# Kernel tuning notes

Hardware: AMD Instinct MI355X
Metric: run time of the kernel (lower is better)

## Reference

```python
import jax, jax.numpy as jnp
import numpy as np

NUM_HEADS = 8
HEAD_SIZE = 64


def setup_inputs() -> dict:
    key = jax.random.key(0)
    ks = jax.random.split(key, 7)
    B, P, De, F = 16, 64, 512, 128
    d_model = NUM_HEADS * HEAD_SIZE  # 512
    s = 0.05  # ~ keras RandomNormal default stddev
    return {
        "patch_embeddings": jax.random.normal(ks[0], (B, P, De), jnp.float32),
        "patches_relative_feature": jax.random.normal(ks[1], (B, P, P, F), jnp.float32),
        "patches_relative_mask": jnp.ones((B, P, P), dtype=bool),
        "Wq": jax.random.normal(ks[2], (De, d_model), jnp.float32) * s,
        "Wk": jax.random.normal(ks[3], (De + F, d_model), jnp.float32) * s,
        "Wv": jax.random.normal(ks[4], (De + F, d_model), jnp.float32) * s,
        "Wo": jax.random.normal(ks[5], (d_model, d_model), jnp.float32) * s,
    }


def reference(patch_embeddings, patches_relative_feature, patches_relative_mask, Wq, Wk, Wv, Wo):
    # Vectorized form of the per-patch python loop: for query patch q,
    # keys/values come from concat(patch_embeddings, rel_feature[:, q]).
    B, P, De = patch_embeddings.shape
    H, hs = NUM_HEADS, HEAD_SIZE
    q = (patch_embeddings @ Wq).reshape(B, P, H, hs)  # [B,P,H,hs], seq_len=1 per patch
    # relative key/value inputs: [B, Pq, Pk, De+F]
    rel = jnp.concatenate(
        [jnp.broadcast_to(patch_embeddings[:, None], (B, P, P, De)), patches_relative_feature],
        axis=-1,
    )
    k = (rel @ Wk).reshape(B, P, P, H, hs)
    v = (rel @ Wv).reshape(B, P, P, H, hs)
    scale = 1.0 / jnp.sqrt(jnp.asarray(hs, q.dtype))
    scores = jnp.einsum("bqhd,bqkhd->bqhk", q, k) * scale  # [B,Pq,H,Pk]
    attn = jax.nn.softmax(scores, axis=-1)
    out = jnp.einsum("bqhk,bqkhd->bqhd", attn, v).reshape(B, P, H * hs)
    return out @ Wo  # [B, P, d_model]
```

## Files before the change

### kernel.cpp

```cpp
#include <hip/hip_runtime.h>
#include <hip/hip_bf16.h>


typedef __attribute__((ext_vector_type(8))) short short8;
typedef __attribute__((ext_vector_type(4))) short short4v;
typedef __attribute__((ext_vector_type(4))) float f32x4;

static __device__ __forceinline__ short f2bf(float x) {
  __hip_bfloat16 h = __float2bfloat16(x);
  union { __hip_bfloat16 h; short s; } u;
  u.h = h;
  return u.s;
}
static __device__ __forceinline__ float bf2f(short s) {
  union { unsigned int u; float f; } c;
  c.u = ((unsigned int)(unsigned short)s) << 16;
  return c.f;
}
static __device__ __forceinline__ float bflo(unsigned int u) {
  union { unsigned int u; float f; } c; c.u = u << 16; return c.f;
}
static __device__ __forceinline__ float bfhi(unsigned int u) {
  union { unsigned int u; float f; } c; c.u = u & 0xFFFF0000u; return c.f;
}
static __device__ __forceinline__ short8 ldcvt(const float* p) {
  float4 v0 = *(const float4*)p, v1 = *(const float4*)(p + 4);
  short8 r = {f2bf(v0.x), f2bf(v0.y), f2bf(v0.z), f2bf(v0.w),
              f2bf(v1.x), f2bf(v1.y), f2bf(v1.z), f2bf(v1.w)};
  return r;
}

__global__ __launch_bounds__(256) void prep(const float* __restrict__ Wq,
                                            const float* __restrict__ Wk,
                                            const float* __restrict__ Wv,
                                            const float* __restrict__ Wo,
                                            short* __restrict__ Bt,
                                            short* __restrict__ BtO,
                                            short* __restrict__ Wk2t,
                                            short* __restrict__ Wv2bf) {
  __shared__ float t[32][33];
  const int bid = blockIdx.x, tid = threadIdx.x;
  if (bid < 1024) {
    const int np0 = (bid & 63) * 32, k0 = (bid >> 6) * 32;
    const int tx = tid & 31, ty = tid >> 5;
    const int sid = np0 >> 9;
    const float* src = (sid == 0) ? Wq : (sid == 1) ? Wv : (sid == 2) ? Wk : Wo;
    const int nc0 = np0 & 511;
#pragma unroll
    for (int r = 0; r < 4; ++r) {
      int kl = ty + r * 8;
      t[kl][tx] = src[(size_t)(k0 + kl) * 512 + nc0 + tx];
    }
    __syncthreads();
#pragma unroll
    for (int r = 0; r < 4; ++r) {
      int nl = ty + r * 8;
      short bv = f2bf(t[tx][nl]);
      int np = np0 + nl;
      if (np < 1536) Bt[(size_t)np * 512 + k0 + tx] = bv;
      else           BtO[(size_t)(np - 1536) * 512 + k0 + tx] = bv;
    }
  } else if (bid < 1088) {
    const int b2 = bid - 1024;
    const int f0 = (b2 & 3) * 32, e0 = (b2 >> 2) * 32;
    const int tx = tid & 31, ty = tid >> 5;
    const float* Wk2 = Wk + 512 * 512;
#pragma unroll
    for (int r = 0; r < 4; ++r) {
      int fl = ty + r * 8;
      t[fl][tx] = Wk2[(size_t)(f0 + fl) * 512 + e0 + tx];
    }
    __syncthreads();
#pragma unroll
    for (int r = 0; r < 4; ++r) {
      int el = ty + r * 8;
      Wk2t[(size_t)(e0 + el) * 128 + f0 + tx] = f2bf(t[tx][el]);
    }
  } else {
    int i = ((bid - 1088) * 256 + tid) * 4;
    const float* Wv2 = Wv + 512 * 512;
    float4 v = *(const float4*)(Wv2 + i);
    short4v o = {f2bf(v.x), f2bf(v.y), f2bf(v.z), f2bf(v.w)};
    *(short4v*)(Wv2bf + i) = o;
  }
}

__global__ __launch_bounds__(256) void gemm_qkvu(const float* __restrict__ A,
                                                 const short* __restrict__ Bt,
                                                 short* __restrict__ QV,
                                                 short* __restrict__ K0t2) {
  const int wave = threadIdx.x >> 6, lane = threadIdx.x & 63;
  const int wr = wave >> 1, wc = wave & 1;
  const int r = lane & 15, g = lane >> 4;
  const int row0 = blockIdx.x * 64 + wr * 32;
  const int col0 = blockIdx.y * 64 + wc * 32;
  const float* a0f = A + (size_t)(row0 + r) * 512 + g * 8;
  const float* a1f = A + (size_t)(row0 + 16 + r) * 512 + g * 8;
  const short8* b0p = (const short8*)(Bt + (size_t)(col0 + r) * 512 + g * 8);
  const short8* b1p = (const short8*)(Bt + (size_t)(col0 + 16 + r) * 512 + g * 8);
  f32x4 acc00 = {}, acc01 = {}, acc10 = {}, acc11 = {};
  short8 A0[2][4], A1[2][4], B0[2][4], B1[2][4];
  auto LOAD = [&](int buf, int ss) {
#pragma unroll
    for (int c = 0; c < 4; ++c) {
      A0[buf][c] = ldcvt(a0f + (ss * 4 + c) * 32);
      A1[buf][c] = ldcvt(a1f + (ss * 4 + c) * 32);
      B0[buf][c] = b0p[(ss * 4 + c) * 4];
      B1[buf][c] = b1p[(ss * 4 + c) * 4];
    }
  };
  auto MM = [&](int buf) {
#pragma unroll
    for (int c = 0; c < 4; ++c) {
      acc00 = __builtin_amdgcn_mfma_f32_16x16x32_bf16(A0[buf][c], B0[buf][c], acc00, 0, 0, 0);
      acc01 = __builtin_amdgcn_mfma_f32_16x16x32_bf16(A0[buf][c], B1[buf][c], acc01, 0, 0, 0);
      acc10 = __builtin_amdgcn_mfma_f32_16x16x32_bf16(A1[buf][c], B0[buf][c], acc10, 0, 0, 0);
      acc11 = __builtin_amdgcn_mfma_f32_16x16x32_bf16(A1[buf][c], B1[buf][c], acc11, 0, 0, 0);
    }
  };
  LOAD(0, 0);
  LOAD(1, 1);
  MM(0);
  LOAD(0, 2);
  MM(1);
  LOAD(1, 3);
  MM(0);
  MM(1);
  const int crow = (lane >> 4) * 4, ccol = lane & 15;
  const bool k0sec = (blockIdx.y >= 16);
#pragma unroll
  for (int i = 0; i < 2; ++i)
#pragma unroll
    for (int j = 0; j < 2; ++j) {
      f32x4 a = (i == 0) ? (j == 0 ? acc00 : acc01) : (j == 0 ? acc10 : acc11);
#pragma unroll
      for (int rg = 0; rg < 4; ++rg) {
        size_t row = row0 + i * 16 + crow + rg;
        size_t col = col0 + j * 16 + ccol;
        short v = f2bf(a[rg]);
        if (!k0sec) {
          QV[row * 1024 + col] = v;
        } else {
          size_t c = col - 1024;
          size_t b = row >> 6, kk = row & 63;
          K0t2[((b * 256 + (c >> 1)) * 64 + kk) * 2 + (c & 1)] = v;
        }
      }
    }
}

__global__ __launch_bounds__(256) void gemm_out(const short* __restrict__ A,
                                                const short* __restrict__ Bt,
                                                float* __restrict__ C) {
  const int wave = threadIdx.x >> 6, lane = threadIdx.x & 63;
  const int wr = wave >> 1, wc = wave & 1;
  const int r = lane & 15, g = lane >> 4;
  const int row0 = blockIdx.x * 64 + wr * 32;
  const int col0 = blockIdx.y * 64 + wc * 32;
  const short8* a0p = (const short8*)(A + (size_t)(row0 + r) * 512 + g * 8);
  const short8* a1p = (const short8*)(A + (size_t)(row0 + 16 + r) * 512 + g * 8);
  const short8* b0p = (const short8*)(Bt + (size_t)(col0 + r) * 512 + g * 8);
  const short8* b1p = (const short8*)(Bt + (size_t)(col0 + 16 + r) * 512 + g * 8);
  f32x4 acc00 = {}, acc01 = {}, acc10 = {}, acc11 = {};
  short8 A0[2][4], A1[2][4], B0[2][4], B1[2][4];
  auto LOAD = [&](int buf, int ss) {
#pragma unroll
    for (int c = 0; c < 4; ++c) {
      A0[buf][c] = a0p[(ss * 4 + c) * 4];
      A1[buf][c] = a1p[(ss * 4 + c) * 4];
      B0[buf][c] = b0p[(ss * 4 + c) * 4];
      B1[buf][c] = b1p[(ss * 4 + c) * 4];
    }
  };
  auto MM = [&](int buf) {
#pragma unroll
    for (int c = 0; c < 4; ++c) {
      acc00 = __builtin_amdgcn_mfma_f32_16x16x32_bf16(A0[buf][c], B0[buf][c], acc00, 0, 0, 0);
      acc01 = __builtin_amdgcn_mfma_f32_16x16x32_bf16(A0[buf][c], B1[buf][c], acc01, 0, 0, 0);
      acc10 = __builtin_amdgcn_mfma_f32_16x16x32_bf16(A1[buf][c], B0[buf][c], acc10, 0, 0, 0);
      acc11 = __builtin_amdgcn_mfma_f32_16x16x32_bf16(A1[buf][c], B1[buf][c], acc11, 0, 0, 0);
    }
  };
  LOAD(0, 0);
  LOAD(1, 1);
  MM(0);
  LOAD(0, 2);
  MM(1);
  LOAD(1, 3);
  MM(0);
  MM(1);
  const int crow = (lane >> 4) * 4, ccol = lane & 15;
#pragma unroll
  for (int i = 0; i < 2; ++i)
#pragma unroll
    for (int j = 0; j < 2; ++j) {
      f32x4 a = (i == 0) ? (j == 0 ? acc00 : acc01) : (j == 0 ? acc10 : acc11);
#pragma unroll
      for (int rg = 0; rg < 4; ++rg)
        C[(size_t)(row0 + i * 16 + crow + rg) * 512 + col0 + j * 16 + ccol] = a[rg];
    }
}

__global__ __launch_bounds__(512) void attn_fused(const short* __restrict__ QV,
                                                  const unsigned int* __restrict__ K0t2,
                                                  const float* __restrict__ relf,
                                                  const short* __restrict__ Wk2t,
                                                  const short* __restrict__ Wv2bf,
                                                  short* __restrict__ AO) {
  const int orig = blockIdx.x;
  const int bq = (orig & 7) * 128 + (orig >> 3);
  const int b = bq >> 6;
  const int tid = threadIdx.x;
  const int h = tid >> 6, lane = tid & 63;

  __shared__ short relf_s[64][136];
  __shared__ float q_s[512];
  __shared__ float u_s[8][128];
  __shared__ float attn_s[8][64];
  __shared__ float w_s[8][128];

  q_s[tid] = bf2f(QV[(size_t)bq * 1024 + tid]);

  const float* rf = relf + (size_t)bq * 8192;
#pragma unroll
  for (int it = 0; it < 4; ++it) {
    int idx = (it * 512 + tid) * 4;
    float4 gv = *(const float4*)(rf + idx);
    int kk = idx >> 7, f = idx & 127;
    short4v o = {f2bf(gv.x), f2bf(gv.y), f2bf(gv.z), f2bf(gv.w)};
    *(short4v*)&relf_s[kk][f] = o;
  }
  __syncthreads();

  {
    const unsigned int* wp = (const unsigned int*)(Wk2t + (size_t)h * 64 * 128) + lane;
    float u0 = 0.f, u1 = 0.f;
#pragma unroll 8
    for (int d = 0; d < 64; ++d) {
      unsigned int uv = wp[d * 64];
      float qd = q_s[h * 64 + d];
      u0 += qd * bflo(uv);
      u1 += qd * bfhi(uv);
    }
    u_s[h][lane * 2] = u0;
    u_s[h][lane * 2 + 1] = u1;
  }

  float s = 0.f;
  {
    const unsigned int* kp = K0t2 + ((size_t)b * 256 + h * 32) * 64 + lane;
#pragma unroll 8
    for (int d2 = 0; d2 < 32; ++d2) {
      unsigned int uv = kp[(size_t)d2 * 64];
      s += q_s[h * 64 + d2 * 2] * bflo(uv) + q_s[h * 64 + d2 * 2 + 1] * bfhi(uv);
    }
#pragma unroll
    for (int f8 = 0; f8 < 16; ++f8) {
      short8 rv = *(const short8*)&relf_s[lane][f8 * 8];
      float4 ua = *(const float4*)&u_s[h][f8 * 8];
      float4 ub = *(const float4*)&u_s[h][f8 * 8 + 4];
      s += ua.x * bf2f(rv[0]) + ua.y * bf2f(rv[1]) + ua.z * bf2f(rv[2]) + ua.w * bf2f(rv[3]);
      s += ub.x * bf2f(rv[4]) + ub.y * bf2f(rv[5]) + ub.z * bf2f(rv[6]) + ub.w * bf2f(rv[7]);
    }
    s *= 0.125f;
  }
  float m = s;
#pragma unroll
  for (int off = 32; off; off >>= 1) m = fmaxf(m, __shfl_xor(m, off));
  float p = __expf(s - m);
  float sum = p;
#pragma unroll
  for (int off = 32; off; off >>= 1) sum += __shfl_xor(sum, off);
  attn_s[h][lane] = p / sum;

  {
    float w0 = 0.f, w1 = 0.f;
#pragma unroll 8
    for (int kk = 0; kk < 64; ++kk) {
      float a = attn_s[h][kk];
      w0 += a * bf2f(relf_s[kk][lane]);
      w1 += a * bf2f(relf_s[kk][lane + 64]);
    }
    w_s[h][lane] = w0;
    w_s[h][lane + 64] = w1;
  }

  float o = 0.f;
  {
    const short* v0col = QV + (size_t)(b * 64) * 1024 + 512 + h * 64 + lane;
#pragma unroll 16
    for (int kk = 0; kk < 64; ++kk) o += attn_s[h][kk] * bf2f(v0col[(size_t)kk * 1024]);
    const short* wvcol = Wv2bf + h * 64 + lane;
#pragma unroll 16
    for (int f = 0; f < 128; ++f) o += w_s[h][f] * bf2f(wvcol[(size_t)f * 512]);
  }
  AO[(size_t)bq * 512 + h * 64 + lane] = f2bf(o);
}

extern "C" void kernel_launch(void* const* d_in, const int* in_sizes, int n_in,
                              void* d_out, int out_size, void* d_ws, size_t ws_size,
                              hipStream_t stream) {
  const float* pe   = (const float*)d_in[0];
  const float* relf = (const float*)d_in[1];
  const float* Wq = (const float*)d_in[3];
  const float* Wk = (const float*)d_in[4];
  const float* Wv = (const float*)d_in[5];
  const float* Wo = (const float*)d_in[6];
  float* out = (float*)d_out;

  short* ws = (short*)d_ws;
  short* Bt    = ws;
  short* BtO   = Bt + 786432;
  short* Wk2t  = BtO + 262144;
  short* Wv2bf = Wk2t + 65536;
  short* QV    = Wv2bf + 65536;
  short* K0t2  = QV + 1048576;
  short* AObf  = K0t2 + 524288;

  prep<<<1152, 256, 0, stream>>>(Wq, Wk, Wv, Wo, Bt, BtO, Wk2t, Wv2bf);
  gemm_qkvu<<<dim3(16, 24), 256, 0, stream>>>(pe, Bt, QV, K0t2);
  attn_fused<<<1024, 512, 0, stream>>>(QV, (const unsigned int*)K0t2, relf, Wk2t, Wv2bf, AObf);
  gemm_out<<<dim3(16, 8), 256, 0, stream>>>(AObf, BtO, out);
}
```

Before: 147.1 us.

## Fuse all four stages into one cooperative persistent kernel with grid syncs

Replaces the four separate launches (weight prep, QKV GEMM, attention, output GEMM) with a single cooperative kernel of 256 blocks that runs each stage in grid-stride loops separated by grid.sync(). The aim is to remove launch overhead and inter-kernel gaps. In exchange it adds grid-wide barriers and gives the attention stage only 256 resident blocks, each looping over 4 queries. The fallback kernels' software-pipelined MFMA loops are also simplified into plain unrolled loops.

```diff
diff --git a/kernel.cpp b/kernel.cpp
--- a/kernel.cpp
+++ b/kernel.cpp
@@ -1,5 +1,8 @@
 #include <hip/hip_runtime.h>
 #include <hip/hip_bf16.h>
+#include <hip/hip_cooperative_groups.h>
+
+namespace cg = cooperative_groups;
 
 
 typedef __attribute__((ext_vector_type(8))) short short8;
@@ -28,6 +31,252 @@
   short8 r = {f2bf(v0.x), f2bf(v0.y), f2bf(v0.z), f2bf(v0.w),
               f2bf(v1.x), f2bf(v1.y), f2bf(v1.z), f2bf(v1.w)};
   return r;
+}
+static __device__ __forceinline__ f32x4 mfma_bf(short8 a, short8 b, f32x4 c) {
+  return __builtin_amdgcn_mfma_f32_16x16x32_bf16(a, b, c, 0, 0, 0);
+}
+
+#define WS_BT    0
+#define WS_BTO   786432
+#define WS_WK2T  (WS_BTO + 262144)
+#define WS_WV2   (WS_WK2T + 65536)
+#define WS_QV    (WS_WV2 + 65536)
+#define WS_K0T2  (WS_QV + 1048576)
+#define WS_AO    (WS_K0T2 + 524288)
+
+__global__ __launch_bounds__(512) void fused_all(const float* __restrict__ pe,
+                                                 const float* __restrict__ relf,
+                                                 const float* __restrict__ Wq,
+                                                 const float* __restrict__ Wk,
+                                                 const float* __restrict__ Wv,
+                                                 const float* __restrict__ Wo,
+                                                 float* __restrict__ out,
+                                                 short* __restrict__ ws) {
+  cg::grid_group grid = cg::this_grid();
+  const int bid = blockIdx.x, tid = threadIdx.x;
+
+  short* Bt    = ws + WS_BT;
+  short* BtO   = ws + WS_BTO;
+  short* Wk2t  = ws + WS_WK2T;
+  short* Wv2bf = ws + WS_WV2;
+  short* QV    = ws + WS_QV;
+  short* K0t2  = ws + WS_K0T2;
+  short* AObf  = ws + WS_AO;
+
+  __shared__ float t[32][33];
+  __shared__ short relf_s[64][136];
+  __shared__ float q_s[512];
+  __shared__ float u_s[8][128];
+  __shared__ float attn_s[8][64];
+  __shared__ float w_s[8][128];
+
+  {
+    const int tx = tid & 31, ty2 = tid >> 5;
+    for (int slot = bid; slot < 1120; slot += 256) {
+      if (slot < 1024) {
+        const int np0 = (slot & 63) * 32, k0 = (slot >> 6) * 32;
+        const int sid = np0 >> 9;
+        const float* src = (sid == 0) ? Wq : (sid == 1) ? Wv : (sid == 2) ? Wk : Wo;
+        const int nc0 = np0 & 511;
+#pragma unroll
+        for (int r = 0; r < 2; ++r) {
+          int kl = ty2 + r * 16;
+          t[kl][tx] = src[(size_t)(k0 + kl) * 512 + nc0 + tx];
+        }
+        __syncthreads();
+#pragma unroll
+        for (int r = 0; r < 2; ++r) {
+          int nl = ty2 + r * 16;
+          short bv = f2bf(t[tx][nl]);
+          int np = np0 + nl;
+          if (np < 1536) Bt[(size_t)np * 512 + k0 + tx] = bv;
+          else           BtO[(size_t)(np - 1536) * 512 + k0 + tx] = bv;
+        }
+        __syncthreads();
+      } else if (slot < 1088) {
+        const int b2 = slot - 1024;
+        const int f0 = (b2 & 3) * 32, e0 = (b2 >> 2) * 32;
+        const float* Wk2 = Wk + 512 * 512;
+#pragma unroll
+        for (int r = 0; r < 2; ++r) {
+          int fl = ty2 + r * 16;
+          t[fl][tx] = Wk2[(size_t)(f0 + fl) * 512 + e0 + tx];
+        }
+        __syncthreads();
+#pragma unroll
+        for (int r = 0; r < 2; ++r) {
+          int el = ty2 + r * 16;
+          Wk2t[(size_t)(e0 + el) * 128 + f0 + tx] = f2bf(t[tx][el]);
+        }
+        __syncthreads();
+      } else {
+        int i = ((slot - 1088) * 512 + tid) * 4;
+        const float* Wv2 = Wv + 512 * 512;
+        float4 v = *(const float4*)(Wv2 + i);
+        short4v o = {f2bf(v.x), f2bf(v.y), f2bf(v.z), f2bf(v.w)};
+        *(short4v*)(Wv2bf + i) = o;
+      }
+    }
+  }
+  grid.sync();
+
+  {
+    const int w = (tid >> 6) & 3, lane = tid & 63;
+    const int r = lane & 15, g = lane >> 4;
+#pragma unroll 1
+    for (int pass = 0; pass < 2; ++pass) {
+      const int unit = pass * 512 + bid * 2 + (tid >> 8);
+      if (unit < 768) {
+        const int m = unit & 31, n = unit >> 5;
+        const int row = m * 32 + (w & 1) * 16 + r;
+        const int col0 = n * 64 + (w >> 1) * 32;
+        const float* af = pe + (size_t)row * 512 + g * 8;
+        const short8* b0p = (const short8*)(Bt + (size_t)(col0 + r) * 512 + g * 8);
+        const short8* b1p = (const short8*)(Bt + (size_t)(col0 + 16 + r) * 512 + g * 8);
+        f32x4 acc0 = {}, acc1 = {};
+#pragma unroll 4
+        for (int tk = 0; tk < 16; ++tk) {
+          short8 a = ldcvt(af + tk * 32);
+          acc0 = mfma_bf(a, b0p[tk * 4], acc0);
+          acc1 = mfma_bf(a, b1p[tk * 4], acc1);
+        }
+        const int crow = (lane >> 4) * 4, ccol = lane & 15;
+#pragma unroll
+        for (int j = 0; j < 2; ++j) {
+          f32x4 fr = j ? acc1 : acc0;
+#pragma unroll
+          for (int rg = 0; rg < 4; ++rg) {
+            size_t orow = (size_t)m * 32 + (w & 1) * 16 + crow + rg;
+            size_t ocol = (size_t)col0 + j * 16 + ccol;
+            short v = f2bf(fr[rg]);
+            if (ocol < 1024) {
+              QV[orow * 1024 + ocol] = v;
+            } else {
+              size_t c = ocol - 1024;
+              K0t2[(((orow >> 6) * 256 + (c >> 1)) * 64 + (orow & 63)) * 2 + (c & 1)] = v;
+            }
+          }
+        }
+      }
+    }
+  }
+  grid.sync();
+
+  {
+    const int h = tid >> 6, lane = tid & 63;
+    const unsigned int* K0t2u = (const unsigned int*)K0t2;
+#pragma unroll 1
+    for (int it = 0; it < 4; ++it) {
+      const int bq = (bid & 7) * 128 + (bid >> 3) + it * 32;
+      const int b = bq >> 6;
+      __syncthreads();
+      q_s[tid] = bf2f(QV[(size_t)bq * 1024 + tid]);
+      const float* rf = relf + (size_t)bq * 8192;
+#pragma unroll
+      for (int i4 = 0; i4 < 4; ++i4) {
+        int idx = (i4 * 512 + tid) * 4;
+        float4 gv = *(const float4*)(rf + idx);
+        int kk = idx >> 7, f = idx & 127;
+        short4v o = {f2bf(gv.x), f2bf(gv.y), f2bf(gv.z), f2bf(gv.w)};
+        *(short4v*)&relf_s[kk][f] = o;
+      }
+      __syncthreads();
+
+      {
+        const unsigned int* wp = (const unsigned int*)(Wk2t + (size_t)h * 64 * 128) + lane;
+        float u0 = 0.f, u1 = 0.f;
+#pragma unroll 8
+        for (int d = 0; d < 64; ++d) {
+          unsigned int uv = wp[d * 64];
+          float qd = q_s[h * 64 + d];
+          u0 += qd * bflo(uv);
+          u1 += qd * bfhi(uv);
+        }
+        u_s[h][lane * 2] = u0;
+        u_s[h][lane * 2 + 1] = u1;
+      }
+
+      float s = 0.f;
+      {
+        const unsigned int* kp = K0t2u + ((size_t)b * 256 + h * 32) * 64 + lane;
+#pragma unroll 8
+        for (int d2 = 0; d2 < 32; ++d2) {
+          unsigned int uv = kp[(size_t)d2 * 64];
+          s += q_s[h * 64 + d2 * 2] * bflo(uv) + q_s[h * 64 + d2 * 2 + 1] * bfhi(uv);
+        }
+#pragma unroll
+        for (int f8 = 0; f8 < 16; ++f8) {
+          short8 rv = *(const short8*)&relf_s[lane][f8 * 8];
+          float4 ua = *(const float4*)&u_s[h][f8 * 8];
+          float4 ub = *(const float4*)&u_s[h][f8 * 8 + 4];
+          s += ua.x * bf2f(rv[0]) + ua.y * bf2f(rv[1]) + ua.z * bf2f(rv[2]) + ua.w * bf2f(rv[3]);
+          s += ub.x * bf2f(rv[4]) + ub.y * bf2f(rv[5]) + ub.z * bf2f(rv[6]) + ub.w * bf2f(rv[7]);
+        }
+        s *= 0.125f;
+      }
+      float mx = s;
+#pragma unroll
+      for (int off = 32; off; off >>= 1) mx = fmaxf(mx, __shfl_xor(mx, off));
+      float p = __expf(s - mx);
+      float sum = p;
+#pragma unroll
+      for (int off = 32; off; off >>= 1) sum += __shfl_xor(sum, off);
+      attn_s[h][lane] = p / sum;
+
+      {
+        float w0 = 0.f, w1 = 0.f;
+#pragma unroll 8
+        for (int kk = 0; kk < 64; ++kk) {
+          float a = attn_s[h][kk];
+          w0 += a * bf2f(relf_s[kk][lane]);
+          w1 += a * bf2f(relf_s[kk][lane + 64]);
+        }
+        w_s[h][lane] = w0;
+        w_s[h][lane + 64] = w1;
+      }
+
+      float o = 0.f;
+      {
+        const short* v0col = QV + (size_t)(b * 64) * 1024 + 512 + h * 64 + lane;
+#pragma unroll 16
+        for (int kk = 0; kk < 64; ++kk) o += attn_s[h][kk] * bf2f(v0col[(size_t)kk * 1024]);
+        const short* wvcol = Wv2bf + h * 64 + lane;
+#pragma unroll 16
+        for (int f = 0; f < 128; ++f) o += w_s[h][f] * bf2f(wvcol[(size_t)f * 512]);
+      }
+      AObf[(size_t)bq * 512 + h * 64 + lane] = f2bf(o);
+    }
+  }
+  grid.sync();
+
+  {
+    const int unit = bid * 2 + (tid >> 8);
+    if (unit < 256) {
+      const int w = (tid >> 6) & 3, lane = tid & 63;
+      const int m = unit & 31, n = unit >> 5;
+      const int r = lane & 15, g = lane >> 4;
+      const int row = m * 32 + (w & 1) * 16 + r;
+      const int col0 = n * 64 + (w >> 1) * 32;
+      const short8* ap = (const short8*)(AObf + (size_t)row * 512 + g * 8);
+      const short8* b0p = (const short8*)(BtO + (size_t)(col0 + r) * 512 + g * 8);
+      const short8* b1p = (const short8*)(BtO + (size_t)(col0 + 16 + r) * 512 + g * 8);
+      f32x4 acc0 = {}, acc1 = {};
+#pragma unroll 4
+      for (int tk = 0; tk < 16; ++tk) {
+        short8 a = ap[tk * 4];
+        acc0 = mfma_bf(a, b0p[tk * 4], acc0);
+        acc1 = mfma_bf(a, b1p[tk * 4], acc1);
+      }
+      const int crow = (lane >> 4) * 4, ccol = lane & 15;
+#pragma unroll
+      for (int j = 0; j < 2; ++j) {
+        f32x4 fr = j ? acc1 : acc0;
+#pragma unroll
+        for (int rg = 0; rg < 4; ++rg)
+          out[(size_t)(m * 32 + (w & 1) * 16 + crow + rg) * 512 + col0 + j * 16 + ccol] = fr[rg];
+      }
+    }
+  }
 }
 
 __global__ __launch_bounds__(256) void prep(const float* __restrict__ Wq,
@@ -99,33 +348,15 @@
   const short8* b0p = (const short8*)(Bt + (size_t)(col0 + r) * 512 + g * 8);
   const short8* b1p = (const short8*)(Bt + (size_t)(col0 + 16 + r) * 512 + g * 8);
   f32x4 acc00 = {}, acc01 = {}, acc10 = {}, acc11 = {};
-  short8 A0[2][4], A1[2][4], B0[2][4], B1[2][4];
-  auto LOAD = [&](int buf, int ss) {
-#pragma unroll
-    for (int c = 0; c < 4; ++c) {
-      A0[buf][c] = ldcvt(a0f + (ss * 4 + c) * 32);
-      A1[buf][c] = ldcvt(a1f + (ss * 4 + c) * 32);
-      B0[buf][c] = b0p[(ss * 4 + c) * 4];
-      B1[buf][c] = b1p[(ss * 4 + c) * 4];
-    }
-  };
-  auto MM = [&](int buf) {
-#pragma unroll
-    for (int c = 0; c < 4; ++c) {
-      acc00 = __builtin_amdgcn_mfma_f32_16x16x32_bf16(A0[buf][c], B0[buf][c], acc00, 0, 0, 0);
-      acc01 = __builtin_amdgcn_mfma_f32_16x16x32_bf16(A0[buf][c], B1[buf][c], acc01, 0, 0, 0);
-      acc10 = __builtin_amdgcn_mfma_f32_16x16x32_bf16(A1[buf][c], B0[buf][c], acc10, 0, 0, 0);
-      acc11 = __builtin_amdgcn_mfma_f32_16x16x32_bf16(A1[buf][c], B1[buf][c], acc11, 0, 0, 0);
-    }
-  };
-  LOAD(0, 0);
-  LOAD(1, 1);
-  MM(0);
-  LOAD(0, 2);
-  MM(1);
-  LOAD(1, 3);
-  MM(0);
-  MM(1);
+#pragma unroll 4
+  for (int t = 0; t < 16; ++t) {
+    short8 a0 = ldcvt(a0f + t * 32), a1 = ldcvt(a1f + t * 32);
+    short8 b0 = b0p[t * 4], b1 = b1p[t * 4];
+    acc00 = mfma_bf(a0, b0, acc00);
+    acc01 = mfma_bf(a0, b1, acc01);
+    acc10 = mfma_bf(a1, b0, acc10);
+    acc11 = mfma_bf(a1, b1, acc11);
+  }
   const int crow = (lane >> 4) * 4, ccol = lane & 15;
   const bool k0sec = (blockIdx.y >= 16);
 #pragma unroll
@@ -162,33 +393,15 @@
   const short8* b0p = (const short8*)(Bt + (size_t)(col0 + r) * 512 + g * 8);
   const short8* b1p = (const short8*)(Bt + (size_t)(col0 + 16 + r) * 512 + g * 8);
   f32x4 acc00 = {}, acc01 = {}, acc10 = {}, acc11 = {};
-  short8 A0[2][4], A1[2][4], B0[2][4], B1[2][4];
-  auto LOAD = [&](int buf, int ss) {
-#pragma unroll
-    for (int c = 0; c < 4; ++c) {
-      A0[buf][c] = a0p[(ss * 4 + c) * 4];
-      A1[buf][c] = a1p[(ss * 4 + c) * 4];
-      B0[buf][c] = b0p[(ss * 4 + c) * 4];
-      B1[buf][c] = b1p[(ss * 4 + c) * 4];
-    }
-  };
-  auto MM = [&](int buf) {
-#pragma unroll
-    for (int c = 0; c < 4; ++c) {
-      acc00 = __builtin_amdgcn_mfma_f32_16x16x32_bf16(A0[buf][c], B0[buf][c], acc00, 0, 0, 0);
-      acc01 = __builtin_amdgcn_mfma_f32_16x16x32_bf16(A0[buf][c], B1[buf][c], acc01, 0, 0, 0);
-      acc10 = __builtin_amdgcn_mfma_f32_16x16x32_bf16(A1[buf][c], B0[buf][c], acc10, 0, 0, 0);
-      acc11 = __builtin_amdgcn_mfma_f32_16x16x32_bf16(A1[buf][c], B1[buf][c], acc11, 0, 0, 0);
-    }
-  };
-  LOAD(0, 0);
-  LOAD(1, 1);
-  MM(0);
-  LOAD(0, 2);
-  MM(1);
-  LOAD(1, 3);
-  MM(0);
-  MM(1);
+#pragma unroll 4
+  for (int t = 0; t < 16; ++t) {
+    short8 a0 = a0p[t * 4], a1 = a1p[t * 4];
+    short8 b0 = b0p[t * 4], b1 = b1p[t * 4];
+    acc00 = mfma_bf(a0, b0, acc00);
+    acc01 = mfma_bf(a0, b1, acc01);
+    acc10 = mfma_bf(a1, b0, acc10);
+    acc11 = mfma_bf(a1, b1, acc11);
+  }
   const int crow = (lane >> 4) * 4, ccol = lane & 15;
 #pragma unroll
   for (int i = 0; i < 2; ++i)
@@ -220,7 +433,6 @@
   __shared__ float w_s[8][128];
 
   q_s[tid] = bf2f(QV[(size_t)bq * 1024 + tid]);
-
   const float* rf = relf + (size_t)bq * 8192;
 #pragma unroll
   for (int it = 0; it < 4; ++it) {
@@ -307,18 +519,23 @@
   const float* Wv = (const float*)d_in[5];
   const float* Wo = (const float*)d_in[6];
   float* out = (float*)d_out;
-
   short* ws = (short*)d_ws;
-  short* Bt    = ws;
-  short* BtO   = Bt + 786432;
-  short* Wk2t  = BtO + 262144;
-  short* Wv2bf = Wk2t + 65536;
-  short* QV    = Wv2bf + 65536;
-  short* K0t2  = QV + 1048576;
-  short* AObf  = K0t2 + 524288;
-
-  prep<<<1152, 256, 0, stream>>>(Wq, Wk, Wv, Wo, Bt, BtO, Wk2t, Wv2bf);
-  gemm_qkvu<<<dim3(16, 24), 256, 0, stream>>>(pe, Bt, QV, K0t2);
-  attn_fused<<<1024, 512, 0, stream>>>(QV, (const unsigned int*)K0t2, relf, Wk2t, Wv2bf, AObf);
-  gemm_out<<<dim3(16, 8), 256, 0, stream>>>(AObf, BtO, out);
-}
+
+  void* args[] = {(void*)&pe, (void*)&relf, (void*)&Wq, (void*)&Wk,
+                  (void*)&Wv, (void*)&Wo, (void*)&out, (void*)&ws};
+  hipError_t err = hipLaunchCooperativeKernel((const void*)fused_all, dim3(256), dim3(512),
+                                              args, 0, stream);
+  if (err != hipSuccess) {
+    short* Bt    = ws + WS_BT;
+    short* BtO   = ws + WS_BTO;
+    short* Wk2t  = ws + WS_WK2T;
+    short* Wv2bf = ws + WS_WV2;
+    short* QV    = ws + WS_QV;
+    short* K0t2  = ws + WS_K0T2;
+    short* AObf  = ws + WS_AO;
+    prep<<<1152, 256, 0, stream>>>(Wq, Wk, Wv, Wo, Bt, BtO, Wk2t, Wv2bf);
+    gemm_qkvu<<<dim3(16, 24), 256, 0, stream>>>(pe, Bt, QV, K0t2);
+    attn_fused<<<1024, 512, 0, stream>>>(QV, (const unsigned int*)K0t2, relf, Wk2t, Wv2bf, AObf);
+    gemm_out<<<dim3(16, 8), 256, 0, stream>>>(AObf, BtO, out);
+  }
+}
```

Result: slower. 277.1 us (+88.4%).

## Fuse output projection into attention kernel and keep relative features in fp32 LDS

Applied to the files above, without the earlier changes.

Drops the separate Wo transpose and MFMA output GEMM. Each attention block now multiplies its 512-wide attention output row by fp32 Wo directly, reading Wo from global memory column-wise. This removes one kernel launch and the bf16 AO round trip, but it re-reads Wo (1 MB) from every one of the 1024 blocks and does that GEMM on scalar FMAs instead of MFMA. Relative features are also stored as fp32 in padded LDS, with no bf16 conversion, and some accumulations are split into several partial sums for ILP.

```diff
diff --git a/kernel.cpp b/kernel.cpp
--- a/kernel.cpp
+++ b/kernel.cpp
@@ -29,22 +29,23 @@
               f2bf(v1.x), f2bf(v1.y), f2bf(v1.z), f2bf(v1.w)};
   return r;
 }
+static __device__ __forceinline__ f32x4 mfma_bf(short8 a, short8 b, f32x4 c) {
+  return __builtin_amdgcn_mfma_f32_16x16x32_bf16(a, b, c, 0, 0, 0);
+}
 
 __global__ __launch_bounds__(256) void prep(const float* __restrict__ Wq,
                                             const float* __restrict__ Wk,
                                             const float* __restrict__ Wv,
-                                            const float* __restrict__ Wo,
                                             short* __restrict__ Bt,
-                                            short* __restrict__ BtO,
                                             short* __restrict__ Wk2t,
                                             short* __restrict__ Wv2bf) {
   __shared__ float t[32][33];
   const int bid = blockIdx.x, tid = threadIdx.x;
-  if (bid < 1024) {
-    const int np0 = (bid & 63) * 32, k0 = (bid >> 6) * 32;
+  if (bid < 768) {
+    const int np0 = (bid % 48) * 32, k0 = (bid / 48) * 32;
     const int tx = tid & 31, ty = tid >> 5;
     const int sid = np0 >> 9;
-    const float* src = (sid == 0) ? Wq : (sid == 1) ? Wv : (sid == 2) ? Wk : Wo;
+    const float* src = (sid == 0) ? Wq : (sid == 1) ? Wv : Wk;
     const int nc0 = np0 & 511;
 #pragma unroll
     for (int r = 0; r < 4; ++r) {
@@ -55,13 +56,10 @@
 #pragma unroll
     for (int r = 0; r < 4; ++r) {
       int nl = ty + r * 8;
-      short bv = f2bf(t[tx][nl]);
-      int np = np0 + nl;
-      if (np < 1536) Bt[(size_t)np * 512 + k0 + tx] = bv;
-      else           BtO[(size_t)(np - 1536) * 512 + k0 + tx] = bv;
-    }
-  } else if (bid < 1088) {
-    const int b2 = bid - 1024;
+      Bt[(size_t)(np0 + nl) * 512 + k0 + tx] = f2bf(t[tx][nl]);
+    }
+  } else if (bid < 832) {
+    const int b2 = bid - 768;
     const int f0 = (b2 & 3) * 32, e0 = (b2 >> 2) * 32;
     const int tx = tid & 31, ty = tid >> 5;
     const float* Wk2 = Wk + 512 * 512;
@@ -77,7 +75,7 @@
       Wk2t[(size_t)(e0 + el) * 128 + f0 + tx] = f2bf(t[tx][el]);
     }
   } else {
-    int i = ((bid - 1088) * 256 + tid) * 4;
+    int i = ((bid - 832) * 256 + tid) * 4;
     const float* Wv2 = Wv + 512 * 512;
     float4 v = *(const float4*)(Wv2 + i);
     short4v o = {f2bf(v.x), f2bf(v.y), f2bf(v.z), f2bf(v.w)};
@@ -112,10 +110,10 @@
   auto MM = [&](int buf) {
 #pragma unroll
     for (int c = 0; c < 4; ++c) {
-      acc00 = __builtin_amdgcn_mfma_f32_16x16x32_bf16(A0[buf][c], B0[buf][c], acc00, 0, 0, 0);
-      acc01 = __builtin_amdgcn_mfma_f32_16x16x32_bf16(A0[buf][c], B1[buf][c], acc01, 0, 0, 0);
-      acc10 = __builtin_amdgcn_mfma_f32_16x16x32_bf16(A1[buf][c], B0[buf][c], acc10, 0, 0, 0);
-      acc11 = __builtin_amdgcn_mfma_f32_16x16x32_bf16(A1[buf][c], B1[buf][c], acc11, 0, 0, 0);
+      acc00 = mfma_bf(A0[buf][c], B0[buf][c], acc00);
+      acc01 = mfma_bf(A0[buf][c], B1[buf][c], acc01);
+      acc10 = mfma_bf(A1[buf][c], B0[buf][c], acc10);
+      acc11 = mfma_bf(A1[buf][c], B1[buf][c], acc11);
     }
   };
   LOAD(0, 0);
@@ -149,75 +147,25 @@
     }
 }
 
-__global__ __launch_bounds__(256) void gemm_out(const short* __restrict__ A,
-                                                const short* __restrict__ Bt,
-                                                float* __restrict__ C) {
-  const int wave = threadIdx.x >> 6, lane = threadIdx.x & 63;
-  const int wr = wave >> 1, wc = wave & 1;
-  const int r = lane & 15, g = lane >> 4;
-  const int row0 = blockIdx.x * 64 + wr * 32;
-  const int col0 = blockIdx.y * 64 + wc * 32;
-  const short8* a0p = (const short8*)(A + (size_t)(row0 + r) * 512 + g * 8);
-  const short8* a1p = (const short8*)(A + (size_t)(row0 + 16 + r) * 512 + g * 8);
-  const short8* b0p = (const short8*)(Bt + (size_t)(col0 + r) * 512 + g * 8);
-  const short8* b1p = (const short8*)(Bt + (size_t)(col0 + 16 + r) * 512 + g * 8);
-  f32x4 acc00 = {}, acc01 = {}, acc10 = {}, acc11 = {};
-  short8 A0[2][4], A1[2][4], B0[2][4], B1[2][4];
-  auto LOAD = [&](int buf, int ss) {
-#pragma unroll
-    for (int c = 0; c < 4; ++c) {
-      A0[buf][c] = a0p[(ss * 4 + c) * 4];
-      A1[buf][c] = a1p[(ss * 4 + c) * 4];
-      B0[buf][c] = b0p[(ss * 4 + c) * 4];
-      B1[buf][c] = b1p[(ss * 4 + c) * 4];
-    }
-  };
-  auto MM = [&](int buf) {
-#pragma unroll
-    for (int c = 0; c < 4; ++c) {
-      acc00 = __builtin_amdgcn_mfma_f32_16x16x32_bf16(A0[buf][c], B0[buf][c], acc00, 0, 0, 0);
-      acc01 = __builtin_amdgcn_mfma_f32_16x16x32_bf16(A0[buf][c], B1[buf][c], acc01, 0, 0, 0);
-      acc10 = __builtin_amdgcn_mfma_f32_16x16x32_bf16(A1[buf][c], B0[buf][c], acc10, 0, 0, 0);
-      acc11 = __builtin_amdgcn_mfma_f32_16x16x32_bf16(A1[buf][c], B1[buf][c], acc11, 0, 0, 0);
-    }
-  };
-  LOAD(0, 0);
-  LOAD(1, 1);
-  MM(0);
-  LOAD(0, 2);
-  MM(1);
-  LOAD(1, 3);
-  MM(0);
-  MM(1);
-  const int crow = (lane >> 4) * 4, ccol = lane & 15;
-#pragma unroll
-  for (int i = 0; i < 2; ++i)
-#pragma unroll
-    for (int j = 0; j < 2; ++j) {
-      f32x4 a = (i == 0) ? (j == 0 ? acc00 : acc01) : (j == 0 ? acc10 : acc11);
-#pragma unroll
-      for (int rg = 0; rg < 4; ++rg)
-        C[(size_t)(row0 + i * 16 + crow + rg) * 512 + col0 + j * 16 + ccol] = a[rg];
-    }
-}
-
-__global__ __launch_bounds__(512) void attn_fused(const short* __restrict__ QV,
-                                                  const unsigned int* __restrict__ K0t2,
-                                                  const float* __restrict__ relf,
-                                                  const short* __restrict__ Wk2t,
-                                                  const short* __restrict__ Wv2bf,
-                                                  short* __restrict__ AO) {
+__global__ __launch_bounds__(512) void attn_out(const short* __restrict__ QV,
+                                                const unsigned int* __restrict__ K0t2,
+                                                const float* __restrict__ relf,
+                                                const short* __restrict__ Wk2t,
+                                                const short* __restrict__ Wv2bf,
+                                                const float* __restrict__ Wo,
+                                                float* __restrict__ out) {
   const int orig = blockIdx.x;
   const int bq = (orig & 7) * 128 + (orig >> 3);
   const int b = bq >> 6;
   const int tid = threadIdx.x;
   const int h = tid >> 6, lane = tid & 63;
 
-  __shared__ short relf_s[64][136];
+  __shared__ float relf_s[64][129];
   __shared__ float q_s[512];
   __shared__ float u_s[8][128];
   __shared__ float attn_s[8][64];
   __shared__ float w_s[8][128];
+  __shared__ float ao_s[512];
 
   q_s[tid] = bf2f(QV[(size_t)bq * 1024 + tid]);
 
@@ -227,8 +175,8 @@
     int idx = (it * 512 + tid) * 4;
     float4 gv = *(const float4*)(rf + idx);
     int kk = idx >> 7, f = idx & 127;
-    short4v o = {f2bf(gv.x), f2bf(gv.y), f2bf(gv.z), f2bf(gv.w)};
-    *(short4v*)&relf_s[kk][f] = o;
+    relf_s[kk][f + 0] = gv.x; relf_s[kk][f + 1] = gv.y;
+    relf_s[kk][f + 2] = gv.z; relf_s[kk][f + 3] = gv.w;
   }
   __syncthreads();
 
@@ -255,12 +203,10 @@
       s += q_s[h * 64 + d2 * 2] * bflo(uv) + q_s[h * 64 + d2 * 2 + 1] * bfhi(uv);
     }
 #pragma unroll
-    for (int f8 = 0; f8 < 16; ++f8) {
-      short8 rv = *(const short8*)&relf_s[lane][f8 * 8];
-      float4 ua = *(const float4*)&u_s[h][f8 * 8];
-      float4 ub = *(const float4*)&u_s[h][f8 * 8 + 4];
-      s += ua.x * bf2f(rv[0]) + ua.y * bf2f(rv[1]) + ua.z * bf2f(rv[2]) + ua.w * bf2f(rv[3]);
-      s += ub.x * bf2f(rv[4]) + ub.y * bf2f(rv[5]) + ub.z * bf2f(rv[6]) + ub.w * bf2f(rv[7]);
+    for (int f4 = 0; f4 < 32; ++f4) {
+      float4 rv = *(const float4*)&relf_s[lane][f4 * 4];
+      const float4 uv = *(const float4*)&u_s[h][f4 * 4];
+      s += uv.x * rv.x + uv.y * rv.y + uv.z * rv.z + uv.w * rv.w;
     }
     s *= 0.125f;
   }
@@ -278,23 +224,42 @@
 #pragma unroll 8
     for (int kk = 0; kk < 64; ++kk) {
       float a = attn_s[h][kk];
-      w0 += a * bf2f(relf_s[kk][lane]);
-      w1 += a * bf2f(relf_s[kk][lane + 64]);
+      w0 += a * relf_s[kk][lane];
+      w1 += a * relf_s[kk][lane + 64];
     }
     w_s[h][lane] = w0;
     w_s[h][lane + 64] = w1;
   }
 
-  float o = 0.f;
-  {
+  {
+    float oa = 0.f, ob = 0.f, oc = 0.f, od = 0.f;
     const short* v0col = QV + (size_t)(b * 64) * 1024 + 512 + h * 64 + lane;
 #pragma unroll 16
-    for (int kk = 0; kk < 64; ++kk) o += attn_s[h][kk] * bf2f(v0col[(size_t)kk * 1024]);
+    for (int kk = 0; kk < 32; ++kk) oa += attn_s[h][kk] * bf2f(v0col[(size_t)kk * 1024]);
+#pragma unroll 16
+    for (int kk = 32; kk < 64; ++kk) ob += attn_s[h][kk] * bf2f(v0col[(size_t)kk * 1024]);
     const short* wvcol = Wv2bf + h * 64 + lane;
 #pragma unroll 16
-    for (int f = 0; f < 128; ++f) o += w_s[h][f] * bf2f(wvcol[(size_t)f * 512]);
-  }
-  AO[(size_t)bq * 512 + h * 64 + lane] = f2bf(o);
+    for (int f = 0; f < 64; ++f) oc += w_s[h][f] * bf2f(wvcol[(size_t)f * 512]);
+#pragma unroll 16
+    for (int f = 64; f < 128; ++f) od += w_s[h][f] * bf2f(wvcol[(size_t)f * 512]);
+    ao_s[h * 64 + lane] = (oa + ob) + (oc + od);
+  }
+  __syncthreads();
+
+  {
+    const float* wcol = Wo + tid;
+    float oa = 0.f, ob = 0.f, oc = 0.f, od = 0.f;
+#pragma unroll 8
+    for (int k = 0; k < 128; ++k) oa += ao_s[k] * wcol[(size_t)k * 512];
+#pragma unroll 8
+    for (int k = 128; k < 256; ++k) ob += ao_s[k] * wcol[(size_t)k * 512];
+#pragma unroll 8
+    for (int k = 256; k < 384; ++k) oc += ao_s[k] * wcol[(size_t)k * 512];
+#pragma unroll 8
+    for (int k = 384; k < 512; ++k) od += ao_s[k] * wcol[(size_t)k * 512];
+    out[(size_t)bq * 512 + tid] = (oa + ob) + (oc + od);
+  }
 }
 
 extern "C" void kernel_launch(void* const* d_in, const int* in_sizes, int n_in,
@@ -310,15 +275,12 @@
 
   short* ws = (short*)d_ws;
   short* Bt    = ws;
-  short* BtO   = Bt + 786432;
-  short* Wk2t  = BtO + 262144;
+  short* Wk2t  = Bt + 786432;
   short* Wv2bf = Wk2t + 65536;
   short* QV    = Wv2bf + 65536;
   short* K0t2  = QV + 1048576;
-  short* AObf  = K0t2 + 524288;
-
-  prep<<<1152, 256, 0, stream>>>(Wq, Wk, Wv, Wo, Bt, BtO, Wk2t, Wv2bf);
+
+  prep<<<896, 256, 0, stream>>>(Wq, Wk, Wv, Bt, Wk2t, Wv2bf);
   gemm_qkvu<<<dim3(16, 24), 256, 0, stream>>>(pe, Bt, QV, K0t2);
-  attn_fused<<<1024, 512, 0, stream>>>(QV, (const unsigned int*)K0t2, relf, Wk2t, Wv2bf, AObf);
-  gemm_out<<<dim3(16, 8), 256, 0, stream>>>(AObf, BtO, out);
-}
+  attn_out<<<1024, 512, 0, stream>>>(QV, (const unsigned int*)K0t2, relf, Wk2t, Wv2bf, Wo, out);
+}
```

After: 177.2 us. 20.5% more time.
